# Kernel tuning notes

Measured on AMD Instinct MI355X. Metric: run time of the kernel, lower is better.

Reference implementation:

```python
import jax, jax.numpy as jnp
import numpy as np

EPS = 1e-5
NUM_HEADS = 16


def rms_norm(x, w):
    v = jnp.mean(x * x, axis=-1, keepdims=True)
    return x * jax.lax.rsqrt(v + EPS) * w


def rotate_half_interleaved(x):
    # pairs (x0,x1) -> (-x1, x0), interleaved layout
    x1 = x[..., 0::2]
    x2 = x[..., 1::2]
    return jnp.stack([-x2, x1], axis=-1).reshape(x.shape)


def setup_inputs() -> dict:
    key = jax.random.key(0)
    ks = jax.random.split(key, 6)
    B, N, C = 2, 2048, 2048
    D = C // NUM_HEADS
    s = 1.0 / np.sqrt(C)
    return {
        "x": jax.random.normal(ks[0], (B, N, C), jnp.float32),
        "w_qkv": jax.random.normal(ks[1], (3 * C, C), jnp.float32) * s,
        "q_norm_w": jnp.ones((C,), jnp.float32),
        "k_norm_w": jnp.ones((C,), jnp.float32),
        "cos": jnp.cos(jax.random.normal(ks[2], (N, D), jnp.float32)),
        "sin": jnp.sin(jax.random.normal(ks[3], (N, D), jnp.float32)),
        "w_proj": jax.random.normal(ks[4], (C, C), jnp.float32) * s,
        "b_proj": jnp.zeros((C,), jnp.float32),
    }


def reference(x, w_qkv, q_norm_w, k_norm_w, cos, sin, w_proj, b_proj):
    B, N, C = x.shape
    H = NUM_HEADS
    D = C // H
    scale = D ** -0.5

    qkv = jnp.einsum("bnc,fc->bnf", x, w_qkv).reshape(B, N, 3, C)
    q, k, v = qkv[:, :, 0], qkv[:, :, 1], qkv[:, :, 2]

    # RMSNorm over full channel dim C (as in the torch module), then head split
    q = rms_norm(q, q_norm_w).reshape(B, N, H, D)
    k = rms_norm(k, k_norm_w).reshape(B, N, H, D)
    v = v.reshape(B, N, H, D)

    # rotary embedding (head_first=False layout [B,N,H,D])
    c = cos[None, :, None, :]
    s = sin[None, :, None, :]
    q = q * c + rotate_half_interleaved(q) * s
    k = k * c + rotate_half_interleaved(k) * s

    attn = jnp.einsum("bnhd,bmhd->bhnm", q, k) * scale  # [B,H,N,N]
    attn = jax.nn.softmax(attn, axis=-1)
    out = jnp.einsum("bhnm,bmhd->bnhd", attn, v).reshape(B, N, C)
    return jnp.einsum("bnc,oc->bno", out, w_proj) + b_proj
```

## Files before the change

### kernel.cpp

```cpp
#include <hip/hip_runtime.h>
#include <stdint.h>

typedef unsigned short u16;
typedef unsigned int   u32;
typedef _Float16 f16_t;
typedef f16_t f16x8 __attribute__((ext_vector_type(8)));
typedef float  f32x4  __attribute__((ext_vector_type(4)));

#define BB 2
#define NN 2048
#define CC 2048
#define HH 16
#define DD 128
#define FF 6144
#define MM 4096

__device__ __forceinline__ u16 f2h(float f){
    f16_t h = (f16_t)f;
    return __builtin_bit_cast(u16, h);
}
__device__ __forceinline__ float h2f(u16 b){
    return (float)__builtin_bit_cast(f16_t, b);
}
__device__ __forceinline__ f32x4 MFMA(f16x8 a, f16x8 b, f32x4 c){
    return __builtin_amdgcn_mfma_f32_16x16x32_f16(a, b, c, 0, 0, 0);
}
__device__ __forceinline__ void gld16(const void* g, void* l){
    __builtin_amdgcn_global_load_lds(
        (const __attribute__((address_space(1))) void*)(g),
        (__attribute__((address_space(3))) void*)(l), 16, 0, 0);
}

__global__ void k_f2h(const float* __restrict__ a, u16* __restrict__ o, int n4){
    int i = blockIdx.x * blockDim.x + threadIdx.x;
    int stride = gridDim.x * blockDim.x;
    for (; i < n4; i += stride){
        float4 v = ((const float4*)a)[i];
        ushort4 r; r.x = f2h(v.x); r.y = f2h(v.y); r.z = f2h(v.z); r.w = f2h(v.w);
        ((ushort4*)o)[i] = r;
    }
}

template<int OUTH>
__global__ __launch_bounds__(256) void k_gemm_bt(
    const u16* __restrict__ A, const u16* __restrict__ Bw,
    float* __restrict__ outf, u16* __restrict__ outb,
    const float* __restrict__ bias, int M, int N, int K)
{
    __shared__ u16 As[2][128 * 32];
    __shared__ u16 Bs[2][128 * 32];
    const int tid  = threadIdx.x;
    const int brow = blockIdx.y * 128;
    const int bcol = blockIdx.x * 128;
    const int w = tid >> 6, lane = tid & 63;
    const int wr = w >> 1, wc = w & 1;
    const int l15 = lane & 15, g = lane >> 4;
    const int sr  = tid >> 2;
    const int scz = ((tid & 3) ^ ((tid >> 3) & 3)) * 8;
    const int gx  = (g ^ ((l15 >> 1) & 3)) * 8;

    f32x4 acc[4][4];
    #pragma unroll
    for (int i = 0; i < 4; i++)
        #pragma unroll
        for (int j = 0; j < 4; j++){
            f32x4 z = {0.f, 0.f, 0.f, 0.f};
            acc[i][j] = z;
        }

    auto stage = [&](int buf, int k0){
        gld16(&Bw[(size_t)(bcol + sr) * K + k0 + scz],      &Bs[buf][w * 512]);
        gld16(&Bw[(size_t)(bcol + sr + 64) * K + k0 + scz], &Bs[buf][2048 + w * 512]);
        gld16(&A [(size_t)(brow + sr) * K + k0 + scz],      &As[buf][w * 512]);
        gld16(&A [(size_t)(brow + sr + 64) * K + k0 + scz], &As[buf][2048 + w * 512]);
    };

    stage(0, 0);
    int cur = 0;
    for (int k0 = 0; k0 < K; k0 += 32){
        __syncthreads();
        if (k0 + 32 < K) stage(cur ^ 1, k0 + 32);
        f16x8 fb[4];
        #pragma unroll
        for (int j = 0; j < 4; j++){
            int row = wc * 64 + j * 16 + l15;
            fb[j] = *(const f16x8*)&Bs[cur][row * 32 + gx];
        }
        #pragma unroll
        for (int i = 0; i < 4; i++){
            int row = wr * 64 + i * 16 + l15;
            f16x8 fa = *(const f16x8*)&As[cur][row * 32 + gx];
            #pragma unroll
            for (int j = 0; j < 4; j++) acc[i][j] = MFMA(fa, fb[j], acc[i][j]);
        }
        cur ^= 1;
    }

    #pragma unroll
    for (int i = 0; i < 4; i++){
        #pragma unroll
        for (int j = 0; j < 4; j++){
            int colg = bcol + wc * 64 + j * 16 + l15;
            #pragma unroll
            for (int r = 0; r < 4; r++){
                int rowg = brow + wr * 64 + i * 16 + 4 * g + r;
                float v = acc[i][j][r];
                if (OUTH) outb[(size_t)rowg * N + colg] = f2h(v);
                else      outf[(size_t)rowg * N + colg] = v + bias[colg];
            }
        }
    }
}

__global__ __launch_bounds__(256) void k_norm_rope(
    const u16* __restrict__ qkv, const float* __restrict__ qw, const float* __restrict__ kw,
    const float* __restrict__ cosb, const float* __restrict__ sinb,
    u16* __restrict__ qout, u16* __restrict__ kout, u16* __restrict__ vout)
{
    const int m = blockIdx.x;
    const int b = m >> 11;
    const int n = m & 2047;
    const int t = threadIdx.x;
    const size_t base = (size_t)m * FF;
    const int e0 = t * 8;
    const float SCL = 0.08838834764831845f * 1.4426950408889634f;

    float qv[8], kvv[8];
    uint4 qa = *(const uint4*)&qkv[base + e0];
    uint4 ka = *(const uint4*)&qkv[base + CC + e0];
    uint4 va = *(const uint4*)&qkv[base + 2 * CC + e0];
    {
        u32 aa[4] = {qa.x, qa.y, qa.z, qa.w};
        u32 bb[4] = {ka.x, ka.y, ka.z, ka.w};
        #pragma unroll
        for (int i = 0; i < 4; i++){
            qv[2*i]   = h2f((u16)(aa[i] & 0xffff));
            qv[2*i+1] = h2f((u16)(aa[i] >> 16));
            kvv[2*i]   = h2f((u16)(bb[i] & 0xffff));
            kvv[2*i+1] = h2f((u16)(bb[i] >> 16));
        }
    }
    float sq = 0.f, sk = 0.f;
    #pragma unroll
    for (int i = 0; i < 8; i++){ sq += qv[i]*qv[i]; sk += kvv[i]*kvv[i]; }
    #pragma unroll
    for (int o = 32; o > 0; o >>= 1){ sq += __shfl_xor(sq, o); sk += __shfl_xor(sk, o); }
    __shared__ float red[8];
    if ((t & 63) == 0){ red[(t >> 6)*2] = sq; red[(t >> 6)*2 + 1] = sk; }
    __syncthreads();
    sq = red[0] + red[2] + red[4] + red[6];
    sk = red[1] + red[3] + red[5] + red[7];
    const float rq = rsqrtf(sq * (1.f / 2048.f) + 1e-5f);
    const float rk = rsqrtf(sk * (1.f / 2048.f) + 1e-5f);

    const int h  = t >> 4;
    const int d0 = (t & 15) * 8;
    const float* cp = cosb + (size_t)n * DD + d0;
    const float* sp = sinb + (size_t)n * DD + d0;
    float qo[8], ko[8];
    #pragma unroll
    for (int j = 0; j < 8; j += 2){
        float c0 = cp[j], c1 = cp[j+1], s0 = sp[j], s1 = sp[j+1];
        float x0 = qv[j]   * rq * qw[e0 + j];
        float x1 = qv[j+1] * rq * qw[e0 + j + 1];
        qo[j]   = (x0 * c0 - x1 * s0) * SCL;
        qo[j+1] = (x1 * c1 + x0 * s1) * SCL;
        float y0 = kvv[j]   * rk * kw[e0 + j];
        float y1 = kvv[j+1] * rk * kw[e0 + j + 1];
        ko[j]   = y0 * c0 - y1 * s0;
        ko[j+1] = y1 * c1 + y0 * s1;
    }
    const size_t obase = ((size_t)(b * HH + h) * NN + n) * DD + d0;
    uint4 pq, pk;
    pq.x = (u32)f2h(qo[0]) | ((u32)f2h(qo[1]) << 16);
    pq.y = (u32)f2h(qo[2]) | ((u32)f2h(qo[3]) << 16);
    pq.z = (u32)f2h(qo[4]) | ((u32)f2h(qo[5]) << 16);
    pq.w = (u32)f2h(qo[6]) | ((u32)f2h(qo[7]) << 16);
    pk.x = (u32)f2h(ko[0]) | ((u32)f2h(ko[1]) << 16);
    pk.y = (u32)f2h(ko[2]) | ((u32)f2h(ko[3]) << 16);
    pk.z = (u32)f2h(ko[4]) | ((u32)f2h(ko[5]) << 16);
    pk.w = (u32)f2h(ko[6]) | ((u32)f2h(ko[7]) << 16);
    *(uint4*)&qout[obase] = pq;
    *(uint4*)&kout[obase] = pk;
    *(uint4*)&vout[obase] = va;
}

__global__ __launch_bounds__(256) void k_vtrans(const u16* __restrict__ V, u16* __restrict__ Vt){
    __shared__ u16 t[64 * 66];
    const int bh = blockIdx.z;
    const int n0 = blockIdx.x * 64, d0 = blockIdx.y * 64;
    const int tid = threadIdx.x;
    const int q = tid & 7, p = tid >> 3;
    #pragma unroll
    for (int it = 0; it < 2; it++){
        int r = p + it * 32;
        const u16* src = V + ((size_t)bh * NN + n0 + r) * DD + d0 + q * 8;
        uint4 v = *(const uint4*)src;
        u32* dst = (u32*)&t[r * 66 + q * 8];
        dst[0] = v.x; dst[1] = v.y; dst[2] = v.z; dst[3] = v.w;
    }
    __syncthreads();
    #pragma unroll
    for (int it = 0; it < 2; it++){
        int rd = p + it * 32;
        u16 o[8];
        #pragma unroll
        for (int j = 0; j < 8; j++) o[j] = t[(q * 8 + j) * 66 + rd];
        *(uint4*)(Vt + ((size_t)bh * DD + d0 + rd) * NN + n0 + q * 8) = *(uint4*)o;
    }
}

__global__ __launch_bounds__(256, 2) void k_attn5(
    const u16* __restrict__ Q, const u16* __restrict__ Kt, const u16* __restrict__ Vt2,
    u16* __restrict__ O)
{
    __shared__ u16 Kbuf[2][8192];
    __shared__ u16 Vbuf[2][8192];
    const int tid = threadIdx.x;
    const int w = tid >> 6, lane = tid & 63;
    const int l15 = lane & 15, g = lane >> 4;
    const int flat = blockIdx.x;
    const int lid  = (flat & 7) * 64 + (flat >> 3);
    const int qb = lid & 15;
    const int h  = (lid >> 4) & 15;
    const int b  = lid >> 8;
    const size_t hb  = (size_t)(b * HH + h) * NN * DD;
    const size_t hbT = (size_t)(b * HH + h) * DD * NN;
    const int qbase = qb * 128 + w * 32;
    const int mperm = 8 * (l15 >> 2) + (l15 & 3);

    f16x8 qf[2][4];
    #pragma unroll
    for (int u = 0; u < 2; u++){
        const u16* qrow = Q + hb + (size_t)(qbase + u * 16 + l15) * DD;
        #pragma unroll
        for (int c = 0; c < 4; c++)
            qf[u][c] = *(const f16x8*)(qrow + c * 32 + 8 * g);
    }

    f32x4 oacc[2][8];
    #pragma unroll
    for (int u = 0; u < 2; u++)
        #pragma unroll
        for (int tb = 0; tb < 8; tb++){ f32x4 z = {0.f,0.f,0.f,0.f}; oacc[u][tb] = z; }
    float lsum0 = 0.f, lsum1 = 0.f;

    auto stage = [&](int buf, int kv0){
        #pragma unroll
        for (int it = 0; it < 8; it++){
            int s = it * 4 + w;
            if (s < 16){
                int hh = s >> 3, t = (s >> 2) & 1, c = s & 3;
                gld16(&Kt[hb + (size_t)(kv0 + 32 * hh + 4 * t + mperm) * DD + 32 * c + 8 * g],
                      &Kbuf[buf][s * 512]);
            } else {
                int s2 = s - 16;
                int hh = s2 >> 3, tb = s2 & 7;
                gld16(&Vt2[hbT + (size_t)(tb * 16 + l15) * NN + kv0 + 32 * hh + 8 * g],
                      &Vbuf[buf][s2 * 512]);
            }
        }
    };

    int cur = 0;
    stage(0, 0);
    for (int kv0 = 0; kv0 < NN; kv0 += 64){
        __syncthreads();
        if (kv0 + 64 < NN) stage(cur ^ 1, kv0 + 64);
        const u16* kb = &Kbuf[cur][0] + lane * 8;
        const u16* vb = &Vbuf[cur][0] + lane * 8;
        #pragma unroll
        for (int hh = 0; hh < 2; hh++){
            f32x4 st00 = {0,0,0,0}, st01 = {0,0,0,0}, st10 = {0,0,0,0}, st11 = {0,0,0,0};
            #pragma unroll
            for (int c = 0; c < 4; c++){
                f16x8 kf0 = *(const f16x8*)(kb + (hh * 8 + c) * 512);
                f16x8 kf1 = *(const f16x8*)(kb + (hh * 8 + 4 + c) * 512);
                st00 = MFMA(kf0, qf[0][c], st00);
                st01 = MFMA(kf0, qf[1][c], st01);
                st10 = MFMA(kf1, qf[0][c], st10);
                st11 = MFMA(kf1, qf[1][c], st11);
            }
            f16x8 pf0, pf1;
            #pragma unroll
            for (int r = 0; r < 4; r++){
                float e00 = exp2f(st00[r]), e10 = exp2f(st10[r]);
                float e01 = exp2f(st01[r]), e11 = exp2f(st11[r]);
                lsum0 += e00 + e10;
                lsum1 += e01 + e11;
                pf0[r] = (f16_t)e00; pf0[r + 4] = (f16_t)e10;
                pf1[r] = (f16_t)e01; pf1[r + 4] = (f16_t)e11;
            }
            #pragma unroll
            for (int tb = 0; tb < 8; tb++){
                f16x8 vf = *(const f16x8*)(vb + (hh * 8 + tb) * 512);
                oacc[0][tb] = MFMA(pf0, vf, oacc[0][tb]);
                oacc[1][tb] = MFMA(pf1, vf, oacc[1][tb]);
            }
        }
        cur ^= 1;
    }

    lsum0 += __shfl_xor(lsum0, 16); lsum0 += __shfl_xor(lsum0, 32);
    lsum1 += __shfl_xor(lsum1, 16); lsum1 += __shfl_xor(lsum1, 32);
    float linv0 = 1.f / lsum0, linv1 = 1.f / lsum1;
    float li0[4], li1[4];
    #pragma unroll
    for (int r = 0; r < 4; r++){
        li0[r] = __shfl(linv0, 4 * g + r);
        li1[r] = __shfl(linv1, 4 * g + r);
    }

    #pragma unroll
    for (int tb = 0; tb < 8; tb++){
        #pragma unroll
        for (int r = 0; r < 4; r++){
            int q0 = qbase + 4 * g + r;
            O[(size_t)(b * NN + q0) * CC + h * DD + tb * 16 + l15] = f2h(oacc[0][tb][r] * li0[r]);
            int q1 = qbase + 16 + 4 * g + r;
            O[(size_t)(b * NN + q1) * CC + h * DD + tb * 16 + l15] = f2h(oacc[1][tb][r] * li1[r]);
        }
    }
}

extern "C" void kernel_launch(void* const* d_in, const int* in_sizes, int n_in,
                              void* d_out, int out_size, void* d_ws, size_t ws_size,
                              hipStream_t stream) {
    const float* x      = (const float*)d_in[0];
    const float* w_qkv  = (const float*)d_in[1];
    const float* qw     = (const float*)d_in[2];
    const float* kw     = (const float*)d_in[3];
    const float* cosb   = (const float*)d_in[4];
    const float* sinb   = (const float*)d_in[5];
    const float* w_proj = (const float*)d_in[6];
    const float* b_proj = (const float*)d_in[7];
    float* out = (float*)d_out;

    const size_t sz_xh   = (size_t)MM * CC * 2;
    const size_t sz_wqkv = (size_t)FF * CC * 2;
    const size_t sz_wprj = (size_t)CC * CC * 2;
    const size_t sz_qkv  = (size_t)MM * FF * 2;
    const size_t sz_t    = (size_t)BB * HH * NN * DD * 2;
    const size_t need = sz_xh + sz_wqkv + sz_wprj + sz_qkv + sz_t*3 + sz_xh;
    if (ws_size < need) return;

    char* ws = (char*)d_ws;
    size_t off = 0;
    auto alloc = [&](size_t bytes){ void* p = ws + off; off += (bytes + 255) & ~(size_t)255; return p; };
    u16* x_h     = (u16*)alloc(sz_xh);
    u16* wqkv_h  = (u16*)alloc(sz_wqkv);
    u16* wprj_h  = (u16*)alloc(sz_wprj);
    u16* qkv     = (u16*)alloc(sz_qkv);
    u16* qr      = (u16*)alloc(sz_t);
    u16* kr      = (u16*)alloc(sz_t);
    u16* vt      = (u16*)alloc(sz_t);
    u16* ob      = (u16*)alloc(sz_xh);
    u16* vt2     = qkv;

    k_f2h<<<2048, 256, 0, stream>>>(x, x_h, MM * CC / 4);
    k_f2h<<<2048, 256, 0, stream>>>(w_qkv, wqkv_h, FF * CC / 4);
    k_f2h<<<1024, 256, 0, stream>>>(w_proj, wprj_h, CC * CC / 4);
    k_gemm_bt<1><<<dim3(FF / 128, MM / 128), 256, 0, stream>>>(
        x_h, wqkv_h, nullptr, qkv, nullptr, MM, FF, CC);
    k_norm_rope<<<MM, 256, 0, stream>>>(qkv, qw, kw, cosb, sinb, qr, kr, vt);
    k_vtrans<<<dim3(NN / 64, DD / 64, BB * HH), 256, 0, stream>>>(vt, vt2);
    k_attn5<<<512, 256, 0, stream>>>(qr, kr, vt2, ob);
    k_gemm_bt<0><<<dim3(CC / 128, MM / 128), 256, 0, stream>>>(
        ob, wprj_h, out, nullptr, b_proj, MM, CC, CC);
}
```

Measured before the change: 326.0 us.

## Triple-buffer GEMM loads, read V directly from qkv, add MFMA priority hints

The GEMM moves from double to triple buffering in LDS, prefetching two K-tiles ahead with explicit vmcnt waits and raw barriers, so global-load latency overlaps with more compute. The norm/rope kernel no longer copies V. The transpose kernel reads V straight from the qkv buffer, which removes one full read and write pass over V. The attention kernel raises wave priority around its MFMA blocks. The extra LDS buffer raises shared memory use per block and could lower occupancy.

```diff
diff --git a/kernel.cpp b/kernel.cpp
--- a/kernel.cpp
+++ b/kernel.cpp
@@ -47,8 +47,8 @@
     float* __restrict__ outf, u16* __restrict__ outb,
     const float* __restrict__ bias, int M, int N, int K)
 {
-    __shared__ u16 As[2][128 * 32];
-    __shared__ u16 Bs[2][128 * 32];
+    __shared__ u16 As[3][128 * 32];
+    __shared__ u16 Bs[3][128 * 32];
     const int tid  = threadIdx.x;
     const int brow = blockIdx.y * 128;
     const int bcol = blockIdx.x * 128;
@@ -76,24 +76,38 @@
     };
 
     stage(0, 0);
-    int cur = 0;
+    stage(1, 32);
+    int c = 0;
     for (int k0 = 0; k0 < K; k0 += 32){
-        __syncthreads();
-        if (k0 + 32 < K) stage(cur ^ 1, k0 + 32);
+        __builtin_amdgcn_sched_barrier(0);
+        __builtin_amdgcn_s_barrier();
+        __builtin_amdgcn_sched_barrier(0);
+        int ct = c + 2; if (ct >= 3) ct -= 3;
+        if (k0 + 64 < K){
+            stage(ct, k0 + 64);
+            asm volatile("s_waitcnt vmcnt(8)" ::: "memory");
+        } else if (k0 + 32 < K){
+            asm volatile("s_waitcnt vmcnt(4)" ::: "memory");
+        } else {
+            asm volatile("s_waitcnt vmcnt(0)" ::: "memory");
+        }
+        __builtin_amdgcn_sched_barrier(0);
+        __builtin_amdgcn_s_barrier();
+        __builtin_amdgcn_sched_barrier(0);
         f16x8 fb[4];
         #pragma unroll
         for (int j = 0; j < 4; j++){
             int row = wc * 64 + j * 16 + l15;
-            fb[j] = *(const f16x8*)&Bs[cur][row * 32 + gx];
+            fb[j] = *(const f16x8*)&Bs[c][row * 32 + gx];
         }
         #pragma unroll
         for (int i = 0; i < 4; i++){
             int row = wr * 64 + i * 16 + l15;
-            f16x8 fa = *(const f16x8*)&As[cur][row * 32 + gx];
+            f16x8 fa = *(const f16x8*)&As[c][row * 32 + gx];
             #pragma unroll
             for (int j = 0; j < 4; j++) acc[i][j] = MFMA(fa, fb[j], acc[i][j]);
         }
-        cur ^= 1;
+        c = (c + 1 == 3) ? 0 : c + 1;
     }
 
     #pragma unroll
@@ -115,7 +129,7 @@
 __global__ __launch_bounds__(256) void k_norm_rope(
     const u16* __restrict__ qkv, const float* __restrict__ qw, const float* __restrict__ kw,
     const float* __restrict__ cosb, const float* __restrict__ sinb,
-    u16* __restrict__ qout, u16* __restrict__ kout, u16* __restrict__ vout)
+    u16* __restrict__ qout, u16* __restrict__ kout)
 {
     const int m = blockIdx.x;
     const int b = m >> 11;
@@ -128,7 +142,6 @@
     float qv[8], kvv[8];
     uint4 qa = *(const uint4*)&qkv[base + e0];
     uint4 ka = *(const uint4*)&qkv[base + CC + e0];
-    uint4 va = *(const uint4*)&qkv[base + 2 * CC + e0];
     {
         u32 aa[4] = {qa.x, qa.y, qa.z, qa.w};
         u32 bb[4] = {ka.x, ka.y, ka.z, ka.w};
@@ -182,19 +195,19 @@
     pk.w = (u32)f2h(ko[6]) | ((u32)f2h(ko[7]) << 16);
     *(uint4*)&qout[obase] = pq;
     *(uint4*)&kout[obase] = pk;
-    *(uint4*)&vout[obase] = va;
-}
-
-__global__ __launch_bounds__(256) void k_vtrans(const u16* __restrict__ V, u16* __restrict__ Vt){
+}
+
+__global__ __launch_bounds__(256) void k_vtrans(const u16* __restrict__ qkv, u16* __restrict__ Vt){
     __shared__ u16 t[64 * 66];
     const int bh = blockIdx.z;
+    const int b = bh >> 4, h = bh & 15;
     const int n0 = blockIdx.x * 64, d0 = blockIdx.y * 64;
     const int tid = threadIdx.x;
     const int q = tid & 7, p = tid >> 3;
     #pragma unroll
     for (int it = 0; it < 2; it++){
         int r = p + it * 32;
-        const u16* src = V + ((size_t)bh * NN + n0 + r) * DD + d0 + q * 8;
+        const u16* src = qkv + (size_t)(b * NN + n0 + r) * FF + 2 * CC + h * DD + d0 + q * 8;
         uint4 v = *(const uint4*)src;
         u32* dst = (u32*)&t[r * 66 + q * 8];
         dst[0] = v.x; dst[1] = v.y; dst[2] = v.z; dst[3] = v.w;
@@ -272,6 +285,7 @@
         #pragma unroll
         for (int hh = 0; hh < 2; hh++){
             f32x4 st00 = {0,0,0,0}, st01 = {0,0,0,0}, st10 = {0,0,0,0}, st11 = {0,0,0,0};
+            __builtin_amdgcn_s_setprio(1);
             #pragma unroll
             for (int c = 0; c < 4; c++){
                 f16x8 kf0 = *(const f16x8*)(kb + (hh * 8 + c) * 512);
@@ -281,6 +295,7 @@
                 st10 = MFMA(kf1, qf[0][c], st10);
                 st11 = MFMA(kf1, qf[1][c], st11);
             }
+            __builtin_amdgcn_s_setprio(0);
             f16x8 pf0, pf1;
             #pragma unroll
             for (int r = 0; r < 4; r++){
@@ -291,12 +306,14 @@
                 pf0[r] = (f16_t)e00; pf0[r + 4] = (f16_t)e10;
                 pf1[r] = (f16_t)e01; pf1[r + 4] = (f16_t)e11;
             }
+            __builtin_amdgcn_s_setprio(1);
             #pragma unroll
             for (int tb = 0; tb < 8; tb++){
                 f16x8 vf = *(const f16x8*)(vb + (hh * 8 + tb) * 512);
                 oacc[0][tb] = MFMA(pf0, vf, oacc[0][tb]);
                 oacc[1][tb] = MFMA(pf1, vf, oacc[1][tb]);
             }
+            __builtin_amdgcn_s_setprio(0);
         }
         cur ^= 1;
     }
@@ -353,17 +370,16 @@
     u16* qkv     = (u16*)alloc(sz_qkv);
     u16* qr      = (u16*)alloc(sz_t);
     u16* kr      = (u16*)alloc(sz_t);
-    u16* vt      = (u16*)alloc(sz_t);
+    u16* vt2     = (u16*)alloc(sz_t);
     u16* ob      = (u16*)alloc(sz_xh);
-    u16* vt2     = qkv;
 
     k_f2h<<<2048, 256, 0, stream>>>(x, x_h, MM * CC / 4);
     k_f2h<<<2048, 256, 0, stream>>>(w_qkv, wqkv_h, FF * CC / 4);
     k_f2h<<<1024, 256, 0, stream>>>(w_proj, wprj_h, CC * CC / 4);
     k_gemm_bt<1><<<dim3(FF / 128, MM / 128), 256, 0, stream>>>(
         x_h, wqkv_h, nullptr, qkv, nullptr, MM, FF, CC);
-    k_norm_rope<<<MM, 256, 0, stream>>>(qkv, qw, kw, cosb, sinb, qr, kr, vt);
-    k_vtrans<<<dim3(NN / 64, DD / 64, BB * HH), 256, 0, stream>>>(vt, vt2);
+    k_norm_rope<<<MM, 256, 0, stream>>>(qkv, qw, kw, cosb, sinb, qr, kr);
+    k_vtrans<<<dim3(NN / 64, DD / 64, BB * HH), 256, 0, stream>>>(qkv, vt2);
     k_attn5<<<512, 256, 0, stream>>>(qr, kr, vt2, ob);
     k_gemm_bt<0><<<dim3(CC / 128, MM / 128), 256, 0, stream>>>(
         ob, wprj_h, out, nullptr, b_proj, MM, CC, CC);
```

New measurement: 318.6 us. 1.02x faster.
